# Performance work log

Hardware: AMD Instinct MI355X
Metric: run time of the kernel (lower is better)

The kernel has to match this reference:

```python
import jax, jax.numpy as jnp
import numpy as np

B_SZ, L, D_MODEL = 2, 1024, 1024
D_INNER, D_STATE, D_CONV = 2048, 16, 4
EPS = 1e-6


def setup_inputs() -> dict:
    key = jax.random.key(0)
    ks = jax.random.split(key, 8)
    def n(k, shape, scale=0.02):
        return jax.random.normal(k, shape, jnp.float32) * scale
    return {
        "x": jax.random.normal(ks[0], (B_SZ, L, D_MODEL), jnp.float32),
        "W_in": n(ks[1], (D_MODEL, 2 * D_INNER)),
        "b_in": jnp.zeros((2 * D_INNER,), jnp.float32),
        "conv_w": n(ks[2], (D_INNER, 1, D_CONV), 0.2),
        "conv_b": jnp.zeros((D_INNER,), jnp.float32),
        "W_xp": n(ks[3], (D_INNER, 2 * D_STATE)),
        "b_xp": jnp.zeros((2 * D_STATE,), jnp.float32),
        "W_dt": n(ks[4], (D_INNER, D_INNER)),
        "b_dt": jnp.full((D_INNER,), -1.0, jnp.float32),
        # torch code does log(randn) (NaN-prone); use log of positive uniform instead
        "A_log": jnp.log(jax.random.uniform(ks[5], (D_INNER, D_STATE), jnp.float32, 0.5, 1.5)),
        "D_skip": jnp.ones((D_INNER,), jnp.float32),
        "W_out": n(ks[6], (D_INNER, D_MODEL)),
        "b_out": jnp.zeros((D_MODEL,), jnp.float32),
        "alpha": jnp.ones((D_MODEL,), jnp.float32),
        "beta": jnp.zeros((D_MODEL,), jnp.float32),
    }


def _selective_scan(xc, delta, A, Bm, Cm, D_skip):
    # xc, delta: (B,L,di); A: (di,ds); Bm, Cm: (B,L,ds)
    dA = jnp.exp(delta[..., None] * A)                     # (B,L,di,ds)
    dBx = (delta * xc)[..., None] * Bm[:, :, None, :]      # (B,L,di,ds)
    h0 = jnp.zeros((xc.shape[0], xc.shape[2], A.shape[1]), xc.dtype)

    def step(h, inp):
        dA_t, dBx_t, C_t = inp
        h = dA_t * h + dBx_t                               # (B,di,ds)
        y_t = jnp.einsum('bds,bs->bd', h, C_t)
        return h, y_t

    _, ys = jax.lax.scan(
        step, h0,
        (dA.transpose(1, 0, 2, 3), dBx.transpose(1, 0, 2, 3), Cm.transpose(1, 0, 2)))
    y = ys.transpose(1, 0, 2)                              # (B,L,di)
    return y + D_skip * xc


def _layernorm(r, alpha, beta):
    # torch LayerNormalization: unbiased std, eps added to std
    mean = jnp.mean(r, axis=-1, keepdims=True)
    diff = r - mean
    var_unb = jnp.sum(diff * diff, axis=-1, keepdims=True) / (r.shape[-1] - 1)
    std = jnp.sqrt(var_unb)
    return alpha * diff / (std + EPS) + beta


def reference(x, W_in, b_in, conv_w, conv_b, W_xp, b_xp, W_dt, b_dt,
              A_log, D_skip, W_out, b_out, alpha, beta):
    residual = x
    xz = x @ W_in + b_in                                   # (B,L,2*di)
    x_in, z = jnp.split(xz, 2, axis=-1)

    # depthwise causal conv1d (torch pads d_conv-1 both sides, slices [:L])
    xt = x_in.transpose(0, 2, 1)                           # (B,di,L)
    xt = jax.lax.conv_general_dilated(
        xt, conv_w, window_strides=(1,), padding=[(D_CONV - 1, 0)],
        feature_group_count=D_INNER, dimension_numbers=('NCH', 'OIH', 'NCH'))
    xt = xt + conv_b[None, :, None]
    x_conv = jax.nn.silu(xt.transpose(0, 2, 1))            # (B,L,di)

    x_proj_out = x_conv @ W_xp + b_xp                      # (B,L,2*ds)
    Bm, Cm = jnp.split(x_proj_out, 2, axis=-1)
    delta = jax.nn.softplus(x_conv @ W_dt + b_dt)          # (B,L,di)
    A = -jnp.exp(A_log)

    y = _selective_scan(x_conv, delta, A, Bm, Cm, D_skip)
    y = y * jax.nn.silu(z)
    out = y @ W_out + b_out                                # (B,L,D)
    return _layernorm(residual + out, alpha, beta)
```

## Files before the change

kernel.cpp:

```cpp
#include <hip/hip_runtime.h>
#include <math.h>

#define B_SZ    2
#define L_SEQ   1024
#define DMODEL  1024
#define DINNER  2048
#define DSTATE  16
#define EPSV    1e-6f

#define CCH 32
#define CS  (L_SEQ / CCH)
#define DT  16

typedef short  bf16x8  __attribute__((ext_vector_type(8)));
typedef float  floatx4 __attribute__((ext_vector_type(4)));
typedef unsigned short ushort8v __attribute__((ext_vector_type(8)));

__device__ __forceinline__ unsigned short f2bf(float f) {
    unsigned int u = __float_as_uint(f);
    unsigned int r = (u + 0x7FFFu + ((u >> 16) & 1u)) >> 16;
    return (unsigned short)r;
}

__device__ __forceinline__ void load16_to_lds(const void* g, void* l) {
    __builtin_amdgcn_global_load_lds(
        (const __attribute__((address_space(1))) void*)g,
        (__attribute__((address_space(3))) void*)l, 16, 0, 0);
}

__global__ __launch_bounds__(256) void cast_bf16_kernel(
    const float* __restrict__ in, unsigned short* __restrict__ out, int n4)
{
    int i = blockIdx.x * 256 + threadIdx.x;
    if (i >= n4) return;
    float4 v = ((const float4*)in)[i];
    ushort4 o = { f2bf(v.x), f2bf(v.y), f2bf(v.z), f2bf(v.w) };
    ((ushort4*)out)[i] = o;
}

__global__ __launch_bounds__(256) void transpose_cast(
    const float* __restrict__ W, unsigned short* __restrict__ Wt, int K, int N)
{
    __shared__ float tile[32][33];
    const int n0 = blockIdx.x * 32;
    const int k0 = blockIdx.y * 32;
    const int c = threadIdx.x & 31;
    const int r = threadIdx.x >> 5;
#pragma unroll
    for (int i = 0; i < 4; ++i)
        tile[r + 8 * i][c] = W[(size_t)(k0 + r + 8 * i) * N + n0 + c];
    __syncthreads();
#pragma unroll
    for (int i = 0; i < 4; ++i)
        Wt[(size_t)(n0 + r + 8 * i) * K + k0 + c] = f2bf(tile[c][r + 8 * i]);
}

template <int TM, int TN, int MODE>
__global__ __launch_bounds__(256) void gemm_bf16(
    const unsigned short* __restrict__ A, const unsigned short* __restrict__ Bt,
    const float* __restrict__ bias, const float* __restrict__ resid,
    float* __restrict__ C, int M, int N, int K)
{
    constexpr int NJ = TN / 32;
    constexpr int WN = TN / 2;
    constexpr int OPW = (TM + TN) / 64;

    __shared__ unsigned short As[2][TM * 32];
    __shared__ unsigned short Bs[2][TN * 32];

    const int tid  = threadIdx.x;
    const int wave = tid >> 6;
    const int lane = tid & 63;
    const int m0 = blockIdx.y * TM;
    const int n0 = blockIdx.x * TN;
    const int wm = (wave >> 1) * 64;
    const int wn = (wave & 1) * WN;

    const int fr = lane & 15;
    const int cq = lane >> 4;
    const int sw = ((fr >> 1) & 3) ^ cq;

    const int srl = lane >> 2;
    const int scg = (lane & 3) ^ ((lane >> 3) & 3);

    auto stage = [&](int bufi, int kt) {
#pragma unroll
        for (int i = 0; i < OPW; ++i) {
            const int o = wave * OPW + i;
            const int row = 16 * o + srl;
            if (16 * o < TM) {
                load16_to_lds(A + (size_t)(m0 + row) * K + kt + scg * 8,
                              &As[bufi][16 * o * 32]);
            } else {
                load16_to_lds(Bt + (size_t)(n0 + row - TM) * K + kt + scg * 8,
                              &Bs[bufi][(16 * o - TM) * 32]);
            }
        }
    };

    floatx4 acc[4][NJ] = {};

    stage(0, 0);
    int buf = 0;
    for (int kt = 0; kt < K; kt += 32) {
        __syncthreads();
        if (kt + 32 < K) stage(buf ^ 1, kt + 32);

        bf16x8 af[4], bfr[NJ];
#pragma unroll
        for (int i = 0; i < 4; ++i)
            af[i] = *(const bf16x8*)&As[buf][(wm + i * 16 + fr) * 32 + sw * 8];
#pragma unroll
        for (int j = 0; j < NJ; ++j)
            bfr[j] = *(const bf16x8*)&Bs[buf][(wn + j * 16 + fr) * 32 + sw * 8];
#pragma unroll
        for (int i = 0; i < 4; ++i)
#pragma unroll
            for (int j = 0; j < NJ; ++j)
                acc[i][j] = __builtin_amdgcn_mfma_f32_16x16x32_bf16(
                    af[i], bfr[j], acc[i][j], 0, 0, 0);
        buf ^= 1;
    }

    const int rq = (lane >> 4) * 4;
#pragma unroll
    for (int i = 0; i < 4; ++i) {
#pragma unroll
        for (int j = 0; j < NJ; ++j) {
            const int col = n0 + wn + j * 16 + fr;
            const float bv = bias[col];
#pragma unroll
            for (int r = 0; r < 4; ++r) {
                const int row = m0 + wm + i * 16 + rq + r;
                float v = acc[i][j][r] + bv;
                if (MODE == 1) {
                    v = (v > 20.f) ? v : log1pf(__expf(v));
                } else if (MODE == 2) {
                    v += resid[(size_t)row * N + col];
                }
                C[(size_t)row * N + col] = v;
            }
        }
    }
}

#define CROWS 4
__global__ __launch_bounds__(256) void conv_xproj(
    const float* __restrict__ xz, const float* __restrict__ conv_w,
    const float* __restrict__ conv_b, const float* __restrict__ W_xp,
    const float* __restrict__ b_xp, float* __restrict__ x_conv,
    unsigned short* __restrict__ x_conv_bf, float* __restrict__ BC)
{
    __shared__ float sxc[CROWS][DINNER];
    __shared__ float red[8][CROWS][32];

    const int tid = threadIdx.x;
    const int r0 = blockIdx.x * CROWS;
    const int c8 = tid * 8;

    float wt[8][4];
#pragma unroll
    for (int ci = 0; ci < 8; ++ci) {
        float4 w4 = *(const float4*)&conv_w[(c8 + ci) * 4];
        wt[ci][0] = w4.x; wt[ci][1] = w4.y; wt[ci][2] = w4.z; wt[ci][3] = w4.w;
    }
    float cb[8];
    *(float4*)&cb[0] = *(const float4*)&conv_b[c8];
    *(float4*)&cb[4] = *(const float4*)&conv_b[c8 + 4];

#pragma unroll
    for (int rr = 0; rr < CROWS; ++rr) {
        const int row = r0 + rr;
        const int l = row & (L_SEQ - 1);
        float acc[8];
#pragma unroll
        for (int ci = 0; ci < 8; ++ci) acc[ci] = cb[ci];
#pragma unroll
        for (int h = 0; h < 4; ++h) {
            const int lsrc = l - 3 + h;
            if (lsrc >= 0) {
                float4 a = *(const float4*)&xz[(size_t)(row - 3 + h) * (2 * DINNER) + c8];
                float4 b = *(const float4*)&xz[(size_t)(row - 3 + h) * (2 * DINNER) + c8 + 4];
                acc[0] += a.x * wt[0][h]; acc[1] += a.y * wt[1][h];
                acc[2] += a.z * wt[2][h]; acc[3] += a.w * wt[3][h];
                acc[4] += b.x * wt[4][h]; acc[5] += b.y * wt[5][h];
                acc[6] += b.z * wt[6][h]; acc[7] += b.w * wt[7][h];
            }
        }
        float o[8];
        ushort8v ob;
#pragma unroll
        for (int ci = 0; ci < 8; ++ci) {
            o[ci] = acc[ci] / (1.f + __expf(-acc[ci]));
            sxc[rr][c8 + ci] = o[ci];
            ob[ci] = (short)f2bf(o[ci]);
        }
        *(float4*)&x_conv[(size_t)row * DINNER + c8]     = *(float4*)&o[0];
        *(float4*)&x_conv[(size_t)row * DINNER + c8 + 4] = *(float4*)&o[4];
        *(ushort8v*)&x_conv_bf[(size_t)row * DINNER + c8] = ob;
    }
    __syncthreads();

    const int n = tid & 31;
    const int g = tid >> 5;
    float p[CROWS] = {};
    const int k0 = g * 256;
#pragma unroll 4
    for (int k = k0; k < k0 + 256; ++k) {
        const float wv = W_xp[k * 32 + n];
        p[0] += sxc[0][k] * wv;
        p[1] += sxc[1][k] * wv;
        p[2] += sxc[2][k] * wv;
        p[3] += sxc[3][k] * wv;
    }
#pragma unroll
    for (int rr = 0; rr < CROWS; ++rr) red[g][rr][n] = p[rr];
    __syncthreads();
    if (tid < CROWS * 32) {
        const int rr = tid >> 5;
        const int n2 = tid & 31;
        float s = b_xp[n2];
#pragma unroll
        for (int gg = 0; gg < 8; ++gg) s += red[gg][rr][n2];
        BC[(size_t)(r0 + rr) * 32 + n2] = s;
    }
}

__global__ __launch_bounds__(512) void scan_kernel(
    const float* __restrict__ delta, const float* __restrict__ x_conv,
    const float* __restrict__ BC, const float* __restrict__ A_log,
    const float* __restrict__ D_skip, const float* __restrict__ xz,
    unsigned short* __restrict__ y_bf)
{
    __shared__ float sA[DSTATE][CCH][DT];
    __shared__ float sH[DSTATE][CCH][DT];

    const int tid = threadIdx.x;
    const int dl  = tid & (DT - 1);
    const int c   = tid >> 4;
    const int b   = blockIdx.x >> 7;
    const int d0  = (blockIdx.x & 127) * DT;
    const int d   = d0 + dl;

    float Al[DSTATE];
#pragma unroll
    for (int s = 0; s < DSTATE; ++s)
        Al[s] = -__expf(A_log[d * DSTATE + s]) * 1.44269504f;
    const float Dsk = D_skip[d];

    float h[DSTATE];
#pragma unroll
    for (int s = 0; s < DSTATE; ++s) h[s] = 0.f;
    float dsum = 0.f;
    const int l0 = c * CS;

    for (int j = 0; j < CS; ++j) {
        const size_t r = (size_t)(b * L_SEQ + l0 + j);
        const float dt = delta[r * DINNER + d];
        const float xc = x_conv[r * DINNER + d];
        float Bv[DSTATE];
        *(float4*)&Bv[0]  = *(const float4*)&BC[r * 32 + 0];
        *(float4*)&Bv[4]  = *(const float4*)&BC[r * 32 + 4];
        *(float4*)&Bv[8]  = *(const float4*)&BC[r * 32 + 8];
        *(float4*)&Bv[12] = *(const float4*)&BC[r * 32 + 12];
        dsum += dt;
        const float dlx = dt * xc;
#pragma unroll
        for (int s = 0; s < DSTATE; ++s) {
            const float e = exp2f(dt * Al[s]);
            h[s] = e * h[s] + dlx * Bv[s];
        }
    }
#pragma unroll
    for (int s = 0; s < DSTATE; ++s) {
        sH[s][c][dl] = h[s];
        sA[s][c][dl] = exp2f(Al[s] * dsum);
    }
    __syncthreads();

    if (tid < DSTATE * DT) {
        const int dl2 = tid & (DT - 1);
        const int s2  = tid >> 4;
        float hh = 0.f;
#pragma unroll
        for (int c2 = 0; c2 < CCH; ++c2) {
            const float a  = sA[s2][c2][dl2];
            const float he = sH[s2][c2][dl2];
            sH[s2][c2][dl2] = hh;
            hh = a * hh + he;
        }
    }
    __syncthreads();

#pragma unroll
    for (int s = 0; s < DSTATE; ++s) h[s] = sH[s][c][dl];

    for (int j = 0; j < CS; ++j) {
        const size_t r = (size_t)(b * L_SEQ + l0 + j);
        const float dt = delta[r * DINNER + d];
        const float xc = x_conv[r * DINNER + d];
        const float z  = xz[r * (2 * DINNER) + DINNER + d];
        float Bv[DSTATE], Cv[DSTATE];
        *(float4*)&Bv[0]  = *(const float4*)&BC[r * 32 + 0];
        *(float4*)&Bv[4]  = *(const float4*)&BC[r * 32 + 4];
        *(float4*)&Bv[8]  = *(const float4*)&BC[r * 32 + 8];
        *(float4*)&Bv[12] = *(const float4*)&BC[r * 32 + 12];
        *(float4*)&Cv[0]  = *(const float4*)&BC[r * 32 + 16];
        *(float4*)&Cv[4]  = *(const float4*)&BC[r * 32 + 20];
        *(float4*)&Cv[8]  = *(const float4*)&BC[r * 32 + 24];
        *(float4*)&Cv[12] = *(const float4*)&BC[r * 32 + 28];
        const float dlx = dt * xc;
        float y = Dsk * xc;
#pragma unroll
        for (int s = 0; s < DSTATE; ++s) {
            const float e = exp2f(dt * Al[s]);
            h[s] = e * h[s] + dlx * Bv[s];
            y += h[s] * Cv[s];
        }
        const float g = z / (1.f + __expf(-z));
        y_bf[r * DINNER + d] = f2bf(y * g);
    }
}

__global__ __launch_bounds__(256) void layernorm_kernel(
    const float* __restrict__ t, const float* __restrict__ alpha,
    const float* __restrict__ beta, float* __restrict__ out)
{
    __shared__ float sred[4];
    __shared__ float sred2[4];
    const int row = blockIdx.x;
    const int tid = threadIdx.x;
    const float* r = t + (size_t)row * DMODEL;

    float4 v = *(const float4*)&r[tid * 4];
    float lsum = v.x + v.y + v.z + v.w;
#pragma unroll
    for (int m = 1; m < 64; m <<= 1) lsum += __shfl_xor(lsum, m);
    if ((tid & 63) == 0) sred[tid >> 6] = lsum;
    __syncthreads();
    const float mean = (sred[0] + sred[1] + sred[2] + sred[3]) * (1.f / DMODEL);

    const float dx = v.x - mean, dy = v.y - mean, dz = v.z - mean, dw = v.w - mean;
    float ls2 = dx * dx + dy * dy + dz * dz + dw * dw;
#pragma unroll
    for (int m = 1; m < 64; m <<= 1) ls2 += __shfl_xor(ls2, m);
    if ((tid & 63) == 0) sred2[tid >> 6] = ls2;
    __syncthreads();
    const float var = (sred2[0] + sred2[1] + sred2[2] + sred2[3]) * (1.f / (DMODEL - 1));
    const float inv = 1.f / (sqrtf(var) + EPSV);

    float4 a4 = *(const float4*)&alpha[tid * 4];
    float4 b4 = *(const float4*)&beta[tid * 4];
    float4 o;
    o.x = a4.x * dx * inv + b4.x;
    o.y = a4.y * dy * inv + b4.y;
    o.z = a4.z * dz * inv + b4.z;
    o.w = a4.w * dw * inv + b4.w;
    *(float4*)&out[(size_t)row * DMODEL + tid * 4] = o;
}

extern "C" void kernel_launch(void* const* d_in, const int* in_sizes, int n_in,
                              void* d_out, int out_size, void* d_ws, size_t ws_size,
                              hipStream_t stream)
{
    const float* x      = (const float*)d_in[0];
    const float* W_in   = (const float*)d_in[1];
    const float* b_in   = (const float*)d_in[2];
    const float* conv_w = (const float*)d_in[3];
    const float* conv_b = (const float*)d_in[4];
    const float* W_xp   = (const float*)d_in[5];
    const float* b_xp   = (const float*)d_in[6];
    const float* W_dt   = (const float*)d_in[7];
    const float* b_dt   = (const float*)d_in[8];
    const float* A_log  = (const float*)d_in[9];
    const float* D_skip = (const float*)d_in[10];
    const float* W_out  = (const float*)d_in[11];
    const float* b_out  = (const float*)d_in[12];
    const float* alpha  = (const float*)d_in[13];
    const float* beta   = (const float*)d_in[14];
    float* out = (float*)d_out;

    const size_t M = (size_t)B_SZ * L_SEQ;
    char* ws = (char*)d_ws;
    float* xz      = (float*)(ws + 0);
    float* x_conv  = (float*)(ws + (32u << 20));
    float* delta   = (float*)(ws + (48u << 20));
    float* BC      = (float*)(ws + (64u << 20));
    unsigned short* x_bf       = (unsigned short*)(ws + (64u << 20) + (512u << 10));
    unsigned short* W_in_t     = (unsigned short*)(ws + (69u << 20));
    unsigned short* W_dt_t     = (unsigned short*)(ws + (77u << 20));
    unsigned short* W_out_t    = (unsigned short*)(ws + (85u << 20));
    unsigned short* x_conv_bf  = (unsigned short*)(ws + (89u << 20));
    unsigned short* ygate_bf   = (unsigned short*)(ws + (77u << 20));
    float* tpre = xz;

    const dim3 blk(256);

    cast_bf16_kernel<<<dim3((unsigned)(M * DMODEL / 4 / 256)), blk, 0, stream>>>(
        x, x_bf, (int)(M * DMODEL / 4));
    transpose_cast<<<dim3(2 * DINNER / 32, DMODEL / 32), blk, 0, stream>>>(
        W_in, W_in_t, DMODEL, 2 * DINNER);
    transpose_cast<<<dim3(DINNER / 32, DINNER / 32), blk, 0, stream>>>(
        W_dt, W_dt_t, DINNER, DINNER);
    transpose_cast<<<dim3(DMODEL / 32, DINNER / 32), blk, 0, stream>>>(
        W_out, W_out_t, DINNER, DMODEL);

    gemm_bf16<128, 128, 0><<<dim3(4096 / 128, 2048 / 128), blk, 0, stream>>>(
        x_bf, W_in_t, b_in, nullptr, xz, 2048, 4096, 1024);

    conv_xproj<<<dim3((unsigned)(M / CROWS)), blk, 0, stream>>>(
        xz, conv_w, conv_b, W_xp, b_xp, x_conv, x_conv_bf, BC);

    gemm_bf16<128, 128, 1><<<dim3(2048 / 128, 2048 / 128), blk, 0, stream>>>(
        x_conv_bf, W_dt_t, b_dt, nullptr, delta, 2048, 2048, 2048);

    scan_kernel<<<dim3(B_SZ * (DINNER / DT)), dim3(512), 0, stream>>>(
        delta, x_conv, BC, A_log, D_skip, xz, ygate_bf);

    gemm_bf16<128, 64, 2><<<dim3(1024 / 64, 2048 / 128), blk, 0, stream>>>(
        ygate_bf, W_out_t, b_out, x, tpre, 2048, 1024, 2048);

    layernorm_kernel<<<dim3((unsigned)M), blk, 0, stream>>>(tpre, alpha, beta, out);
}
```

Measured before the change: 314.6 us.

## Rework bf16 GEMM to register-prefetched single LDS buffer with BK=64 and smaller tiles

Replaces the direct global-to-LDS async loads with double buffering by a scheme that prefetches the next K-tile into registers, computes from a single XOR-swizzled LDS buffer with a K-step of 64, and then writes the prefetched tile to LDS. Tile sizes shrink (128x64 for the in and dt projections, 64x64 for the out projection) and launch bounds ask for 3 blocks per CU, to raise block count and occupancy on the many CUs. The trade-off is two barriers per iteration, more register pressure, and less reuse per block from the smaller tiles.

```diff
diff --git a/kernel.cpp b/kernel.cpp
--- a/kernel.cpp
+++ b/kernel.cpp
@@ -22,12 +22,6 @@
     return (unsigned short)r;
 }
 
-__device__ __forceinline__ void load16_to_lds(const void* g, void* l) {
-    __builtin_amdgcn_global_load_lds(
-        (const __attribute__((address_space(1))) void*)g,
-        (__attribute__((address_space(3))) void*)l, 16, 0, 0);
-}
-
 __global__ __launch_bounds__(256) void cast_bf16_kernel(
     const float* __restrict__ in, unsigned short* __restrict__ out, int n4)
 {
@@ -56,75 +50,98 @@
 }
 
 template <int TM, int TN, int MODE>
-__global__ __launch_bounds__(256) void gemm_bf16(
+__global__ __launch_bounds__(256, 3) void gemm_bf16(
     const unsigned short* __restrict__ A, const unsigned short* __restrict__ Bt,
     const float* __restrict__ bias, const float* __restrict__ resid,
     float* __restrict__ C, int M, int N, int K)
 {
+    constexpr int MI = TM / 32;
     constexpr int NJ = TN / 32;
-    constexpr int WN = TN / 2;
-    constexpr int OPW = (TM + TN) / 64;
-
-    __shared__ unsigned short As[2][TM * 32];
-    __shared__ unsigned short Bs[2][TN * 32];
+    constexpr int NLOAD = (TM + TN) / 32;
+
+    __shared__ unsigned short As[TM * 64];
+    __shared__ unsigned short Bs[TN * 64];
 
     const int tid  = threadIdx.x;
     const int wave = tid >> 6;
     const int lane = tid & 63;
     const int m0 = blockIdx.y * TM;
     const int n0 = blockIdx.x * TN;
-    const int wm = (wave >> 1) * 64;
-    const int wn = (wave & 1) * WN;
-
+    const int wm = (wave >> 1) * (TM / 2);
+    const int wn = (wave & 1) * (TN / 2);
     const int fr = lane & 15;
-    const int cq = lane >> 4;
-    const int sw = ((fr >> 1) & 3) ^ cq;
-
-    const int srl = lane >> 2;
-    const int scg = (lane & 3) ^ ((lane >> 3) & 3);
-
-    auto stage = [&](int bufi, int kt) {
-#pragma unroll
-        for (int i = 0; i < OPW; ++i) {
-            const int o = wave * OPW + i;
-            const int row = 16 * o + srl;
-            if (16 * o < TM) {
-                load16_to_lds(A + (size_t)(m0 + row) * K + kt + scg * 8,
-                              &As[bufi][16 * o * 32]);
-            } else {
-                load16_to_lds(Bt + (size_t)(n0 + row - TM) * K + kt + scg * 8,
-                              &Bs[bufi][(16 * o - TM) * 32]);
+    const int kg = lane >> 4;
+
+    int offs[NLOAD];
+    unsigned short* lp[NLOAD];
+#pragma unroll
+    for (int i = 0; i < NLOAD; ++i) {
+        const int slot = i * 256 + tid;
+        const int row  = slot >> 3;
+        const int ch   = slot & 7;
+        const int pos  = ch ^ (row & 7);
+        if (i < TM / 32) {
+            offs[i] = (m0 + row) * K + ch * 8;
+            lp[i]   = &As[row * 64 + pos * 8];
+        } else {
+            const int rb = row - TM;
+            offs[i] = (n0 + rb) * K + ch * 8;
+            lp[i]   = &Bs[rb * 64 + pos * 8];
+        }
+    }
+
+    floatx4 acc[MI][NJ] = {};
+    bf16x8 pre[NLOAD];
+
+#pragma unroll
+    for (int i = 0; i < NLOAD; ++i)
+        pre[i] = *(const bf16x8*)((i < TM / 32 ? A : Bt) + offs[i]);
+#pragma unroll
+    for (int i = 0; i < NLOAD; ++i)
+        *(bf16x8*)lp[i] = pre[i];
+    __syncthreads();
+
+    for (int kt = 0; kt < K; kt += 64) {
+        const bool more = (kt + 64) < K;
+        if (more) {
+#pragma unroll
+            for (int i = 0; i < NLOAD; ++i)
+                pre[i] = *(const bf16x8*)((i < TM / 32 ? A : Bt) + offs[i] + kt + 64);
+        }
+
+#pragma unroll
+        for (int ks = 0; ks < 2; ++ks) {
+            const int cq = (ks << 2) | kg;
+            bf16x8 af[MI], bfv[NJ];
+#pragma unroll
+            for (int i = 0; i < MI; ++i) {
+                const int row = wm + i * 16 + fr;
+                af[i] = *(const bf16x8*)&As[row * 64 + ((cq ^ (row & 7)) << 3)];
             }
-        }
-    };
-
-    floatx4 acc[4][NJ] = {};
-
-    stage(0, 0);
-    int buf = 0;
-    for (int kt = 0; kt < K; kt += 32) {
+#pragma unroll
+            for (int j = 0; j < NJ; ++j) {
+                const int row = wn + j * 16 + fr;
+                bfv[j] = *(const bf16x8*)&Bs[row * 64 + ((cq ^ (row & 7)) << 3)];
+            }
+#pragma unroll
+            for (int i = 0; i < MI; ++i)
+#pragma unroll
+                for (int j = 0; j < NJ; ++j)
+                    acc[i][j] = __builtin_amdgcn_mfma_f32_16x16x32_bf16(
+                        af[i], bfv[j], acc[i][j], 0, 0, 0);
+        }
         __syncthreads();
-        if (kt + 32 < K) stage(buf ^ 1, kt + 32);
-
-        bf16x8 af[4], bfr[NJ];
-#pragma unroll
-        for (int i = 0; i < 4; ++i)
-            af[i] = *(const bf16x8*)&As[buf][(wm + i * 16 + fr) * 32 + sw * 8];
-#pragma unroll
-        for (int j = 0; j < NJ; ++j)
-            bfr[j] = *(const bf16x8*)&Bs[buf][(wn + j * 16 + fr) * 32 + sw * 8];
-#pragma unroll
-        for (int i = 0; i < 4; ++i)
-#pragma unroll
-            for (int j = 0; j < NJ; ++j)
-                acc[i][j] = __builtin_amdgcn_mfma_f32_16x16x32_bf16(
-                    af[i], bfr[j], acc[i][j], 0, 0, 0);
-        buf ^= 1;
+        if (more) {
+#pragma unroll
+            for (int i = 0; i < NLOAD; ++i)
+                *(bf16x8*)lp[i] = pre[i];
+        }
+        __syncthreads();
     }
 
     const int rq = (lane >> 4) * 4;
 #pragma unroll
-    for (int i = 0; i < 4; ++i) {
+    for (int i = 0; i < MI; ++i) {
 #pragma unroll
         for (int j = 0; j < NJ; ++j) {
             const int col = n0 + wn + j * 16 + fr;
@@ -405,19 +422,19 @@
     transpose_cast<<<dim3(DMODEL / 32, DINNER / 32), blk, 0, stream>>>(
         W_out, W_out_t, DINNER, DMODEL);
 
-    gemm_bf16<128, 128, 0><<<dim3(4096 / 128, 2048 / 128), blk, 0, stream>>>(
+    gemm_bf16<128, 64, 0><<<dim3(4096 / 64, 2048 / 128), blk, 0, stream>>>(
         x_bf, W_in_t, b_in, nullptr, xz, 2048, 4096, 1024);
 
     conv_xproj<<<dim3((unsigned)(M / CROWS)), blk, 0, stream>>>(
         xz, conv_w, conv_b, W_xp, b_xp, x_conv, x_conv_bf, BC);
 
-    gemm_bf16<128, 128, 1><<<dim3(2048 / 128, 2048 / 128), blk, 0, stream>>>(
+    gemm_bf16<128, 64, 1><<<dim3(2048 / 64, 2048 / 128), blk, 0, stream>>>(
         x_conv_bf, W_dt_t, b_dt, nullptr, delta, 2048, 2048, 2048);
 
     scan_kernel<<<dim3(B_SZ * (DINNER / DT)), dim3(512), 0, stream>>>(
         delta, x_conv, BC, A_log, D_skip, xz, ygate_bf);
 
-    gemm_bf16<128, 64, 2><<<dim3(1024 / 64, 2048 / 128), blk, 0, stream>>>(
+    gemm_bf16<64, 64, 2><<<dim3(1024 / 64, 2048 / 64), blk, 0, stream>>>(
         ygate_bf, W_out_t, b_out, x, tpre, 2048, 1024, 2048);
 
     layernorm_kernel<<<dim3((unsigned)M), blk, 0, stream>>>(tpre, alpha, beta, out);
```

Result: faster. 299.3 us (-4.8%).
